# Kernel optimization log

Measured on AMD Instinct MI355X. Metric: run time of the kernel, lower is better.

The kernel has to match this reference:

```python
import jax, jax.numpy as jnp
import numpy as np

D_MODEL = 1024
N_EXPERTS = 8
TOP_K = 2
LN_EPS = 1e-5


def setup_inputs() -> dict:
    key = jax.random.key(0)
    ks = jax.random.split(key, 8)
    B, S, d, E = 2, 2048, D_MODEL, N_EXPERTS
    f = 2 * d
    s_in = 0.02
    return {
        "x": jax.random.normal(ks[0], (B, S, d), jnp.float32),
        "Wg": jax.random.normal(ks[1], (d, E), jnp.float32) * s_in,
        "bg": jnp.zeros((E,), jnp.float32),
        "W1": jax.random.normal(ks[2], (E, d, f), jnp.float32) * s_in,
        "b1": jnp.zeros((E, f), jnp.float32),
        "W2": jax.random.normal(ks[3], (E, f, d), jnp.float32) * s_in,
        "b2": jnp.zeros((E, d), jnp.float32),
        "gamma": jnp.ones((d,), jnp.float32),
        "beta": jnp.zeros((d,), jnp.float32),
    }


def reference(x, Wg, bg, W1, b1, W2, b2, gamma, beta):
    # Gating + top-k routing (softmax over the selected top-k logits only)
    logits = jnp.einsum("bsd,de->bse", x, Wg) + bg            # [B,S,E]
    topk_vals, topk_idx = jax.lax.top_k(logits, TOP_K)         # [B,S,K]
    topk_w = jax.nn.softmax(topk_vals, axis=-1)                # [B,S,K]

    # Expert MLPs evaluated densely for all experts (dropout is identity in eval)
    h = jax.nn.relu(jnp.einsum("bsd,edf->bsef", x, W1) + b1)   # [B,S,E,2d]
    eo = jnp.einsum("bsef,efd->bsed", h, W2) + b2              # [B,S,E,d]

    # Gather the top-k experts' outputs per token and combine with gate weights
    sel = jnp.take_along_axis(eo, topk_idx[..., None], axis=2)  # [B,S,K,d]
    mixed = jnp.sum(sel * topk_w[..., None], axis=2)            # [B,S,d]

    # Residual + LayerNorm
    y = mixed + x
    mu = jnp.mean(y, axis=-1, keepdims=True)
    var = jnp.mean(jnp.square(y - mu), axis=-1, keepdims=True)
    return gamma * (y - mu) * jax.lax.rsqrt(var + LN_EPS) + beta
```

## Files before the change

### kernel.cpp

```cpp
#include <hip/hip_runtime.h>


typedef unsigned short ushort_t;
typedef short short8 __attribute__((ext_vector_type(8)));
typedef float f32x4 __attribute__((ext_vector_type(4)));

#define T_TOKENS 4096
#define DMODEL 1024
#define FFN 2048
#define NEXP 8
#define MAXSLOTS 9216
#define GATE_BLOCKS 1024
#define TOK_PER_BLK 4
#define MAX_MT 12

__device__ __forceinline__ ushort_t f2bf(float f) {
    unsigned u = __float_as_uint(f);
    return (ushort_t)((u + 0x7fffu + ((u >> 16) & 1u)) >> 16);
}
__device__ __forceinline__ float bflo(unsigned packed) {
    return __uint_as_float(packed << 16);
}
__device__ __forceinline__ float bfhi(unsigned packed) {
    return __uint_as_float(packed & 0xffff0000u);
}

__device__ __forceinline__ void gload_lds16(const void* g, void* l) {
    __builtin_amdgcn_global_load_lds(
        (const __attribute__((address_space(1))) unsigned int*)g,
        (__attribute__((address_space(3))) unsigned int*)l,
        16, 0, 0);
}

__global__ __launch_bounds__(256) void gate_kernel(
    const float* __restrict__ x, const float* __restrict__ Wg,
    const float* __restrict__ bg,
    int* __restrict__ top_idx, float* __restrict__ top_w,
    int* __restrict__ blk_hist)
{
    __shared__ int hist[NEXP];
    const int tid = threadIdx.x, lane = tid & 63, w = tid >> 6;
    if (tid < NEXP) hist[tid] = 0;
    __syncthreads();

    const int t = blockIdx.x * TOK_PER_BLK + w;
    const float* xr = x + (size_t)t * DMODEL;
    float acc[8] = {0.f,0.f,0.f,0.f,0.f,0.f,0.f,0.f};
    #pragma unroll
    for (int i = 0; i < 16; i++) {
        float xv = xr[i * 64 + lane];
        const float4* wp = (const float4*)&Wg[(i * 64 + lane) * 8];
        float4 a = wp[0], b = wp[1];
        acc[0] += xv * a.x; acc[1] += xv * a.y;
        acc[2] += xv * a.z; acc[3] += xv * a.w;
        acc[4] += xv * b.x; acc[5] += xv * b.y;
        acc[6] += xv * b.z; acc[7] += xv * b.w;
    }
    #pragma unroll
    for (int off = 32; off > 0; off >>= 1) {
        #pragma unroll
        for (int e = 0; e < 8; e++) acc[e] += __shfl_down(acc[e], off);
    }
    if (lane == 0) {
        float l[8];
        #pragma unroll
        for (int e = 0; e < 8; e++) l[e] = acc[e] + bg[e];
        int i0 = 0; float v0 = l[0];
        #pragma unroll
        for (int e = 1; e < 8; e++) if (l[e] > v0) { v0 = l[e]; i0 = e; }
        int i1 = -1; float v1 = -1e30f;
        #pragma unroll
        for (int e = 0; e < 8; e++) if (e != i0 && l[e] > v1) { v1 = l[e]; i1 = e; }
        float eg = expf(v1 - v0);
        float den = 1.f + eg;
        int p0 = atomicAdd(&hist[i0], 1);
        int p1 = atomicAdd(&hist[i1], 1);
        top_idx[2 * t]     = i0 | (p0 << 4);
        top_idx[2 * t + 1] = i1 | (p1 << 4);
        top_w[2 * t]     = 1.f / den;
        top_w[2 * t + 1] = eg / den;
    }
    __syncthreads();
    if (tid < NEXP) blk_hist[blockIdx.x * NEXP + tid] = hist[tid];
}

__global__ __launch_bounds__(512) void scan_kernel(
    const int* __restrict__ blk_hist, int* __restrict__ blk_base,
    int* __restrict__ offs)
{
    __shared__ int cnt[NEXP];
    const int tid = threadIdx.x, lane = tid & 63, e = tid >> 6;
    int orig[GATE_BLOCKS / 64];
    #pragma unroll
    for (int r = 0; r < GATE_BLOCKS / 64; r++)
        orig[r] = blk_hist[(r * 64 + lane) * NEXP + e];
    int carry = 0;
    #pragma unroll
    for (int r = 0; r < GATE_BLOCKS / 64; r++) {
        int v = orig[r];
        #pragma unroll
        for (int off = 1; off < 64; off <<= 1) {
            int u = __shfl_up(v, off);
            if (lane >= off) v += u;
        }
        blk_base[(r * 64 + lane) * NEXP + e] = carry + v - orig[r];
        carry += __shfl(v, 63);
    }
    if (lane == 0) cnt[e] = carry;
    __syncthreads();
    if (tid == 0) {
        int cum = 0;
        for (int ee = 0; ee < NEXP; ee++) {
            offs[ee] = cum;
            cum += (cnt[ee] + 127) & ~127;
        }
        offs[NEXP] = cum;
    }
}

__global__ __launch_bounds__(256) void scatter_gather_kernel(
    const float* __restrict__ x, const int* __restrict__ top_idx,
    const int* __restrict__ offs, const int* __restrict__ blk_base,
    int* __restrict__ slot_of, ushort_t* __restrict__ Xg)
{
    const int t = blockIdx.x, tid = threadIdx.x;
    __shared__ int slots[2];
    if (tid < 2) {
        int v = top_idx[2 * t + tid];
        int e = v & 15, pos = v >> 4;
        int gb = t / TOK_PER_BLK;
        int slot = offs[e] + blk_base[gb * NEXP + e] + pos;
        slot_of[2 * t + tid] = slot;
        slots[tid] = slot;
    }
    __syncthreads();
    float4 xv = ((const float4*)(x + (size_t)t * DMODEL))[tid];
    uint2 pk;
    pk.x = f2bf(xv.x) | ((unsigned)f2bf(xv.y) << 16);
    pk.y = f2bf(xv.z) | ((unsigned)f2bf(xv.w) << 16);
    ((uint2*)(Xg + (size_t)slots[0] * DMODEL))[tid] = pk;
    ((uint2*)(Xg + (size_t)slots[1] * DMODEL))[tid] = pk;
}

__global__ __launch_bounds__(256) void transpose_kernel(
    const float* __restrict__ W1, const float* __restrict__ W2,
    ushort_t* __restrict__ W1T, ushort_t* __restrict__ W2T)
{
    int b = blockIdx.x;
    const float* s; ushort_t* d; int Rs, Cs, rt, ct;
    if (b < 4096) {
        int e = b >> 9, t = b & 511;
        rt = t >> 5; ct = t & 31;
        s = W1 + (size_t)e * DMODEL * FFN;
        d = W1T + (size_t)e * DMODEL * FFN;
        Rs = DMODEL; Cs = FFN;
    } else {
        b -= 4096;
        int e = b >> 9, t = b & 511;
        rt = t >> 4; ct = t & 15;
        s = W2 + (size_t)e * DMODEL * FFN;
        d = W2T + (size_t)e * DMODEL * FFN;
        Rs = FFN; Cs = DMODEL;
    }
    const int r0 = rt * 64, c0 = ct * 64;
    const int tid = threadIdx.x;

    __shared__ float tile[64][65];

    {
        const int r  = tid >> 4;
        const int c4 = (tid & 15) * 4;
        #pragma unroll
        for (int p = 0; p < 4; p++) {
            float4 v = *(const float4*)&s[(size_t)(r0 + p * 16 + r) * Cs + c0 + c4];
            tile[p * 16 + r][c4 + 0] = v.x;
            tile[p * 16 + r][c4 + 1] = v.y;
            tile[p * 16 + r][c4 + 2] = v.z;
            tile[p * 16 + r][c4 + 3] = v.w;
        }
    }
    __syncthreads();

    {
        const int c  = tid >> 2;
        const int rb = (tid & 3) * 8;
        uint4 o0, o1;
        {
            unsigned p0 = (unsigned)f2bf(tile[rb + 0][c]) | ((unsigned)f2bf(tile[rb + 1][c]) << 16);
            unsigned p1 = (unsigned)f2bf(tile[rb + 2][c]) | ((unsigned)f2bf(tile[rb + 3][c]) << 16);
            unsigned p2 = (unsigned)f2bf(tile[rb + 4][c]) | ((unsigned)f2bf(tile[rb + 5][c]) << 16);
            unsigned p3 = (unsigned)f2bf(tile[rb + 6][c]) | ((unsigned)f2bf(tile[rb + 7][c]) << 16);
            o0.x = p0; o0.y = p1; o0.z = p2; o0.w = p3;
        }
        {
            unsigned p0 = (unsigned)f2bf(tile[rb + 32][c]) | ((unsigned)f2bf(tile[rb + 33][c]) << 16);
            unsigned p1 = (unsigned)f2bf(tile[rb + 34][c]) | ((unsigned)f2bf(tile[rb + 35][c]) << 16);
            unsigned p2 = (unsigned)f2bf(tile[rb + 36][c]) | ((unsigned)f2bf(tile[rb + 37][c]) << 16);
            unsigned p3 = (unsigned)f2bf(tile[rb + 38][c]) | ((unsigned)f2bf(tile[rb + 39][c]) << 16);
            o1.x = p0; o1.y = p1; o1.z = p2; o1.w = p3;
        }
        ushort_t* drow = d + (size_t)(c0 + c) * Rs + r0;
        *(uint4*)&drow[rb]      = o0;
        *(uint4*)&drow[rb + 32] = o1;
    }
}

template <int K, int N, bool RELU>
__global__ __launch_bounds__(256) void expert_gemm(
    const ushort_t* __restrict__ A,
    const ushort_t* __restrict__ Bt,
    const float* __restrict__ bias,
    ushort_t* __restrict__ Cout,
    const int* __restrict__ offs)
{
    const int e  = blockIdx.x;
    const int nt = blockIdx.y;
    const int mt = blockIdx.z;
    const int off_e = offs[e];
    const int Mpad  = offs[e + 1] - off_e;
    if (mt * 128 >= Mpad) return;

    __shared__ __align__(16) ushort_t As[128 * 32];
    __shared__ __align__(16) ushort_t Bs[128 * 32];

    const int tid  = threadIdx.x;
    const int lane = tid & 63;
    const int w    = tid >> 6;
    const int quad = lane >> 4;
    const int r16  = lane & 15;
    const int lrow = lane >> 2;
    const int lk   = (((lane & 3) ^ ((lane >> 3) & 3))) * 8;

    const size_t arow0 = (size_t)(off_e + mt * 128);
    const ushort_t* aS0 = A + (arow0 + (size_t)(2 * w + 0) * 16 + lrow) * K + lk;
    const ushort_t* aS1 = A + (arow0 + (size_t)(2 * w + 1) * 16 + lrow) * K + lk;
    const ushort_t* Bte = Bt + (size_t)e * N * K;
    const ushort_t* bS0 = Bte + ((size_t)(nt * 128 + (2 * w + 0) * 16 + lrow)) * K + lk;
    const ushort_t* bS1 = Bte + ((size_t)(nt * 128 + (2 * w + 1) * 16 + lrow)) * K + lk;
    ushort_t* aD0 = &As[(2 * w + 0) * 512];
    ushort_t* aD1 = &As[(2 * w + 1) * 512];
    ushort_t* bD0 = &Bs[(2 * w + 0) * 512];
    ushort_t* bD1 = &Bs[(2 * w + 1) * 512];

    const int wm = (w >> 1) * 64;
    const int wn = (w & 1) * 64;
    const int sw = ((r16 >> 1) & 3) ^ quad;

    f32x4 acc[4][4];
    #pragma unroll
    for (int i = 0; i < 4; i++)
        #pragma unroll
        for (int j = 0; j < 4; j++)
            acc[i][j] = (f32x4){0.f, 0.f, 0.f, 0.f};

    for (int k0 = 0; k0 < K; k0 += 32) {
        gload_lds16(aS0 + k0, aD0);
        gload_lds16(aS1 + k0, aD1);
        gload_lds16(bS0 + k0, bD0);
        gload_lds16(bS1 + k0, bD1);
        __syncthreads();
        short8 af[4], bfr[4];
        #pragma unroll
        for (int i = 0; i < 4; i++)
            af[i] = *(const short8*)&As[(wm + i * 16 + r16) * 32 + sw * 8];
        #pragma unroll
        for (int j = 0; j < 4; j++)
            bfr[j] = *(const short8*)&Bs[(wn + j * 16 + r16) * 32 + sw * 8];
        #pragma unroll
        for (int i = 0; i < 4; i++)
            #pragma unroll
            for (int j = 0; j < 4; j++)
                acc[i][j] = __builtin_amdgcn_mfma_f32_16x16x32_bf16(
                    af[i], bfr[j], acc[i][j], 0, 0, 0);
        __syncthreads();
    }

    const float* be = bias + (size_t)e * N;
    #pragma unroll
    for (int i = 0; i < 4; i++) {
        #pragma unroll
        for (int j = 0; j < 4; j++) {
            int n = nt * 128 + wn + j * 16 + r16;
            float bv = be[n];
            #pragma unroll
            for (int r = 0; r < 4; r++) {
                int m = mt * 128 + wm + i * 16 + quad * 4 + r;
                float v = acc[i][j][r] + bv;
                if (RELU) v = v > 0.f ? v : 0.f;
                Cout[(size_t)(off_e + m) * N + n] = f2bf(v);
            }
        }
    }
}

__global__ __launch_bounds__(256) void ln_kernel(
    const float* __restrict__ x, const ushort_t* __restrict__ O,
    const int* __restrict__ slot_of, const float* __restrict__ top_w,
    const float* __restrict__ gamma, const float* __restrict__ beta,
    float* __restrict__ out)
{
    int t = blockIdx.x, tid = threadIdx.x;
    int s0 = slot_of[2 * t], s1 = slot_of[2 * t + 1];
    float w0 = top_w[2 * t], w1 = top_w[2 * t + 1];
    float4 xv = ((const float4*)(x + (size_t)t * DMODEL))[tid];
    uint2 a = ((const uint2*)(O + (size_t)s0 * DMODEL))[tid];
    uint2 b = ((const uint2*)(O + (size_t)s1 * DMODEL))[tid];

    float y[4];
    y[0] = xv.x + w0 * bflo(a.x) + w1 * bflo(b.x);
    y[1] = xv.y + w0 * bfhi(a.x) + w1 * bfhi(b.x);
    y[2] = xv.z + w0 * bflo(a.y) + w1 * bflo(b.y);
    y[3] = xv.w + w0 * bfhi(a.y) + w1 * bfhi(b.y);

    float s = y[0] + y[1] + y[2] + y[3];
    float sq = y[0]*y[0] + y[1]*y[1] + y[2]*y[2] + y[3]*y[3];
    __shared__ float red[2][4];
    #pragma unroll
    for (int off = 32; off > 0; off >>= 1) {
        s += __shfl_down(s, off);
        sq += __shfl_down(sq, off);
    }
    int lane = tid & 63, wv = tid >> 6;
    if (lane == 0) { red[0][wv] = s; red[1][wv] = sq; }
    __syncthreads();
    if (tid == 0) {
        float S = red[0][0] + red[0][1] + red[0][2] + red[0][3];
        float SQ = red[1][0] + red[1][1] + red[1][2] + red[1][3];
        float mu = S * (1.f / DMODEL);
        float var = SQ * (1.f / DMODEL) - mu * mu;
        red[0][0] = mu;
        red[1][0] = rsqrtf(var + 1e-5f);
    }
    __syncthreads();
    float mu = red[0][0], inv = red[1][0];
    float4 gv = ((const float4*)gamma)[tid];
    float4 bv = ((const float4*)beta)[tid];
    float4 ov;
    ov.x = gv.x * (y[0] - mu) * inv + bv.x;
    ov.y = gv.y * (y[1] - mu) * inv + bv.y;
    ov.z = gv.z * (y[2] - mu) * inv + bv.z;
    ov.w = gv.w * (y[3] - mu) * inv + bv.w;
    ((float4*)(out + (size_t)t * DMODEL))[tid] = ov;
}

extern "C" void kernel_launch(void* const* d_in, const int* in_sizes, int n_in,
                              void* d_out, int out_size, void* d_ws, size_t ws_size,
                              hipStream_t stream)
{
    const float* x     = (const float*)d_in[0];
    const float* Wg    = (const float*)d_in[1];
    const float* bg    = (const float*)d_in[2];
    const float* W1    = (const float*)d_in[3];
    const float* b1    = (const float*)d_in[4];
    const float* W2    = (const float*)d_in[5];
    const float* b2    = (const float*)d_in[6];
    const float* gamma = (const float*)d_in[7];
    const float* beta  = (const float*)d_in[8];
    float* out = (float*)d_out;

    char* ws = (char*)d_ws;
    size_t o = 0;
    auto alloc = [&](size_t bytes) {
        size_t r = o;
        o = (o + bytes + 255) & ~(size_t)255;
        return r;
    };
    size_t o_offs    = alloc((NEXP + 1) * 4);
    size_t o_topidx  = alloc((size_t)T_TOKENS * 2 * 4);
    size_t o_topw    = alloc((size_t)T_TOKENS * 2 * 4);
    size_t o_slotof  = alloc((size_t)T_TOKENS * 2 * 4);
    size_t o_bhist   = alloc((size_t)GATE_BLOCKS * NEXP * 4);
    size_t o_bbase   = alloc((size_t)GATE_BLOCKS * NEXP * 4);
    size_t o_w1t     = alloc((size_t)NEXP * DMODEL * FFN * 2);
    size_t o_w2t     = alloc((size_t)NEXP * DMODEL * FFN * 2);
    size_t o_xg      = alloc((size_t)MAXSLOTS * DMODEL * 2);
    size_t o_h       = alloc((size_t)MAXSLOTS * FFN * 2);
    size_t o_obuf    = alloc((size_t)MAXSLOTS * DMODEL * 2);
    (void)ws_size; (void)in_sizes; (void)n_in; (void)out_size;

    int*      offs     = (int*)(ws + o_offs);
    int*      top_idx  = (int*)(ws + o_topidx);
    float*    top_w    = (float*)(ws + o_topw);
    int*      slot_of  = (int*)(ws + o_slotof);
    int*      blk_hist = (int*)(ws + o_bhist);
    int*      blk_base = (int*)(ws + o_bbase);
    ushort_t* W1T      = (ushort_t*)(ws + o_w1t);
    ushort_t* W2T      = (ushort_t*)(ws + o_w2t);
    ushort_t* Xg       = (ushort_t*)(ws + o_xg);
    ushort_t* H        = (ushort_t*)(ws + o_h);
    ushort_t* Obuf     = (ushort_t*)(ws + o_obuf);

    gate_kernel<<<GATE_BLOCKS, 256, 0, stream>>>(x, Wg, bg, top_idx, top_w, blk_hist);
    transpose_kernel<<<8192, 256, 0, stream>>>(W1, W2, W1T, W2T);
    scan_kernel<<<1, 512, 0, stream>>>(blk_hist, blk_base, offs);
    scatter_gather_kernel<<<T_TOKENS, 256, 0, stream>>>(x, top_idx, offs, blk_base, slot_of, Xg);
    expert_gemm<DMODEL, FFN, true>
        <<<dim3(NEXP, FFN / 128, MAX_MT), 256, 0, stream>>>(Xg, W1T, b1, H, offs);
    expert_gemm<FFN, DMODEL, false>
        <<<dim3(NEXP, DMODEL / 128, MAX_MT), 256, 0, stream>>>(H, W2T, b2, Obuf, offs);
    ln_kernel<<<T_TOKENS, 256, 0, stream>>>(x, Obuf, slot_of, top_w, gamma, beta, out);
}
```

Before: 319.6 us.

## Double-buffer expert GEMM LDS tiles and use direct-to-LDS loads in transpose

```diff
diff --git a/kernel.cpp b/kernel.cpp
--- a/kernel.cpp
+++ b/kernel.cpp
@@ -164,20 +164,15 @@
     }
     const int r0 = rt * 64, c0 = ct * 64;
     const int tid = threadIdx.x;
-
-    __shared__ float tile[64][65];
-
-    {
-        const int r  = tid >> 4;
-        const int c4 = (tid & 15) * 4;
-        #pragma unroll
-        for (int p = 0; p < 4; p++) {
-            float4 v = *(const float4*)&s[(size_t)(r0 + p * 16 + r) * Cs + c0 + c4];
-            tile[p * 16 + r][c4 + 0] = v.x;
-            tile[p * 16 + r][c4 + 1] = v.y;
-            tile[p * 16 + r][c4 + 2] = v.z;
-            tile[p * 16 + r][c4 + 3] = v.w;
-        }
+    const int w = tid >> 6, lane = tid & 63;
+
+    __shared__ __align__(16) float tile[64][64];
+
+    #pragma unroll
+    for (int p = 0; p < 4; p++) {
+        const float* src =
+            &s[(size_t)(r0 + p * 16 + w * 4 + (lane >> 4)) * Cs + c0 + (lane & 15) * 4];
+        gload_lds16(src, &tile[p * 16 + w * 4][0]);
     }
     __syncthreads();
 
@@ -220,8 +215,8 @@
     const int Mpad  = offs[e + 1] - off_e;
     if (mt * 128 >= Mpad) return;
 
-    __shared__ __align__(16) ushort_t As[128 * 32];
-    __shared__ __align__(16) ushort_t Bs[128 * 32];
+    __shared__ __align__(16) ushort_t As[2][128 * 32];
+    __shared__ __align__(16) ushort_t Bs[2][128 * 32];
 
     const int tid  = threadIdx.x;
     const int lane = tid & 63;
@@ -237,10 +232,6 @@
     const ushort_t* Bte = Bt + (size_t)e * N * K;
     const ushort_t* bS0 = Bte + ((size_t)(nt * 128 + (2 * w + 0) * 16 + lrow)) * K + lk;
     const ushort_t* bS1 = Bte + ((size_t)(nt * 128 + (2 * w + 1) * 16 + lrow)) * K + lk;
-    ushort_t* aD0 = &As[(2 * w + 0) * 512];
-    ushort_t* aD1 = &As[(2 * w + 1) * 512];
-    ushort_t* bD0 = &Bs[(2 * w + 0) * 512];
-    ushort_t* bD1 = &Bs[(2 * w + 1) * 512];
 
     const int wm = (w >> 1) * 64;
     const int wn = (w & 1) * 64;
@@ -253,25 +244,37 @@
         for (int j = 0; j < 4; j++)
             acc[i][j] = (f32x4){0.f, 0.f, 0.f, 0.f};
 
-    for (int k0 = 0; k0 < K; k0 += 32) {
-        gload_lds16(aS0 + k0, aD0);
-        gload_lds16(aS1 + k0, aD1);
-        gload_lds16(bS0 + k0, bD0);
-        gload_lds16(bS1 + k0, bD1);
-        __syncthreads();
+    auto stage = [&](int b, int k0) {
+        gload_lds16(aS0 + k0, &As[b][(2 * w + 0) * 512]);
+        gload_lds16(aS1 + k0, &As[b][(2 * w + 1) * 512]);
+        gload_lds16(bS0 + k0, &Bs[b][(2 * w + 0) * 512]);
+        gload_lds16(bS1 + k0, &Bs[b][(2 * w + 1) * 512]);
+    };
+    auto compute = [&](int b) {
         short8 af[4], bfr[4];
         #pragma unroll
         for (int i = 0; i < 4; i++)
-            af[i] = *(const short8*)&As[(wm + i * 16 + r16) * 32 + sw * 8];
+            af[i] = *(const short8*)&As[b][(wm + i * 16 + r16) * 32 + sw * 8];
         #pragma unroll
         for (int j = 0; j < 4; j++)
-            bfr[j] = *(const short8*)&Bs[(wn + j * 16 + r16) * 32 + sw * 8];
+            bfr[j] = *(const short8*)&Bs[b][(wn + j * 16 + r16) * 32 + sw * 8];
         #pragma unroll
         for (int i = 0; i < 4; i++)
             #pragma unroll
             for (int j = 0; j < 4; j++)
                 acc[i][j] = __builtin_amdgcn_mfma_f32_16x16x32_bf16(
                     af[i], bfr[j], acc[i][j], 0, 0, 0);
+    };
+
+    stage(0, 0);
+    __syncthreads();
+    #pragma unroll 1
+    for (int k0 = 0; k0 < K; k0 += 64) {
+        if (k0 + 32 < K) stage(1, k0 + 32);
+        compute(0);
+        __syncthreads();
+        if (k0 + 64 < K) stage(0, k0 + 64);
+        compute(1);
         __syncthreads();
     }
 
```

After: 367.1 us. +14.9%, slower.
